# Performance work log

Hardware: AMD Instinct MI355X
Metric: run time of the kernel (lower is better)

## Reference

```python
import jax, jax.numpy as jnp
import numpy as np

# module config (matches init_kwargs)
EMBED = 128; HEADS = 8; HEAD_DIM = EMBED // HEADS  # 16, power of 2
MODES = 16            # hardcoded in FuncSelfAttention
WS = 4                # window_size
SHIFT = 2             # shift_size
NSUB = 8              # n_sub (subdomain grid of the full image)
NW = (NSUB // WS) ** 2   # 4 windows per image
S = WS * WS              # 16 tokens (subdomains) per window
BATCH0 = 4; B = BATCH0 * NW  # 16
P = 32                # per-subdomain spatial resolution (needs P//2+1 >= MODES)
HID = 512             # LogCPB MLP hidden width (Swin-v2 style)


def win_decompose2d(x, nsx, nsy, ws):
    # x: [b, c, H, W] -> [(b*wx*wy), ws*ws, c, sh, sw]
    b, c, H, W = x.shape
    sh = H // nsx; sw = W // nsy
    wx = nsx // ws; wy = nsy // ws
    x = x.reshape(b, c, wx, ws, sh, wy, ws, sw)
    x = x.transpose(0, 2, 5, 3, 6, 1, 4, 7)  # b, wx, wy, qx, qy, c, sh, sw
    return x.reshape(b * wx * wy, ws * ws, c, sh, sw)


def win_recompose2d(x, nsx, nsy, ws):
    # inverse of win_decompose2d: [(b*wx*wy), ws*ws, c, sh, sw] -> [b, c, H, W]
    wx = nsx // ws; wy = nsy // ws
    Bn, s, c, sh, sw = x.shape
    b = Bn // (wx * wy)
    x = x.reshape(b, wx, wy, ws, ws, c, sh, sw)
    x = x.transpose(0, 5, 1, 3, 6, 2, 4, 7)
    return x.reshape(b, c, wx * ws * sh, wy * ws * sw)


def spectral_conv(x, wr, wi):
    # SimpleSpectralConv2d: rfft2 -> low-mode complex channel mixing -> irfft2
    # x: [b, s, cin, h, w]; wr/wi: [cin, cout, m, m]
    m = wr.shape[-1]
    h, w = x.shape[-2:]
    xf = jnp.fft.rfft2(x, axes=(-2, -1))                       # [b,s,cin,h,w//2+1]
    ym = jnp.einsum('bsixy,ioxy->bsoxy', xf[..., :m, :m], wr + 1j * wi)
    out_ft = jnp.zeros(x.shape[:2] + (wr.shape[1], h, w // 2 + 1), dtype=ym.dtype)
    out_ft = out_ft.at[..., :m, :m].set(ym)
    return jnp.fft.irfft2(out_ft, s=(h, w), axes=(-2, -1))


def log_cpb(ws, w1, b1, w2):
    # Swin-v2 style log-spaced continuous position bias MLP -> [heads, S, S]
    g = jnp.arange(ws)
    coords = jnp.stack(jnp.meshgrid(g, g, indexing='ij'), -1).reshape(-1, 2)  # [S,2]
    rel = (coords[:, None, :] - coords[None, :, :]).astype(jnp.float32)       # [S,S,2]
    rel = jnp.sign(rel) * jnp.log2(1.0 + jnp.abs(rel)) / jnp.log2(8.0) * 8.0
    hdn = jax.nn.relu(rel @ w1 + b1)
    return (hdn @ w2).transpose(2, 0, 1)


def _build_attn_mask():
    # Faithful port of the Swin shifted-window mask construction in __init__
    img = np.zeros((NSUB, NSUB), np.float32)
    sl = [slice(0, -WS), slice(-WS, -SHIFT), slice(-SHIFT, None)]
    cnt = 0
    for hs in sl:
        for ws_ in sl:
            img[hs, ws_] = cnt
            cnt += 1
    mw = img.reshape(NSUB // WS, WS, NSUB // WS, WS).transpose(0, 2, 1, 3).reshape(NW, S)
    diff = mw[:, None, :] - mw[:, :, None]
    m = np.where(diff != 0, -1e9, 0.0).astype(np.float32)      # -inf in torch; -1e9 for safe grads
    return np.broadcast_to(m[:, None, :, :], (NW, HEADS, S, S)).copy()


def setup_inputs():
    key = jax.random.key(0)
    ks = jax.random.split(key, 8)
    sc = 1.0 / EMBED
    return {
        'seq': jax.random.normal(ks[0], (B, S, EMBED, P, P), jnp.float32),
        'qkv_wr': jax.random.normal(ks[1], (EMBED, 3 * EMBED, MODES, MODES), jnp.float32) * sc,
        'qkv_wi': jax.random.normal(ks[2], (EMBED, 3 * EMBED, MODES, MODES), jnp.float32) * sc,
        'out_wr': jax.random.normal(ks[3], (EMBED, EMBED, MODES, MODES), jnp.float32) * sc,
        'out_wi': jax.random.normal(ks[4], (EMBED, EMBED, MODES, MODES), jnp.float32) * sc,
        'cpb_w1': jax.random.normal(ks[5], (2, HID), jnp.float32) * 0.1,
        'cpb_b1': jnp.zeros((HID,), jnp.float32),
        'cpb_w2': jax.random.normal(ks[6], (HID, HEADS), jnp.float32) * 0.05,
        'attn_mask': jnp.asarray(_build_attn_mask()),
    }


def reference(seq, qkv_wr, qkv_wi, out_wr, out_wi, cpb_w1, cpb_b1, cpb_w2, attn_mask):
    Bn, s, C, h, w = seq.shape
    ssx = w // WS; ssy = h // WS  # subdomain_size per code: seq.size(-1)//n_sub_x with n_sub_x=window_size
    # shift: recompose windows to images, roll, decompose back
    x = win_recompose2d(seq, WS, WS, WS)
    x = jnp.roll(x, (-SHIFT * ssx, -SHIFT * ssy), axis=(-2, -1))
    x = win_decompose2d(x, WS, WS, WS)
    # qkv = spectral conv + residual tiling (v.repeat with dims[2]=3)
    qkv = spectral_conv(x, qkv_wr, qkv_wi) + jnp.concatenate([x, x, x], axis=2)
    qkv = qkv.reshape(Bn, s, 3, HEADS, HEAD_DIM, h, w)
    q = qkv[:, :, 0].transpose(0, 2, 1, 3, 4, 5)  # [B, H, s, d, h, w]
    k = qkv[:, :, 1].transpose(0, 2, 1, 3, 4, 5)
    v = qkv[:, :, 2].transpose(0, 2, 1, 3, 4, 5)
    bias = attn_mask + log_cpb(WS, cpb_w1, cpb_b1, cpb_w2)[None]  # [nW, H, S, S]
    # 'reimann' scores: Riemann-sum (mean over grid) inner product of q_i, k_j functions
    scale = 1.0 / ((h * w) * jnp.sqrt(jnp.float32(HEAD_DIM)))
    scores = jnp.einsum('bnidxy,bnjdxy->bnij', q, k) * scale      # [B, H, S, S]
    scores = scores.reshape(Bn // NW, NW, HEADS, s, s) + bias[None]
    attn = jax.nn.softmax(scores, axis=-1).reshape(Bn, HEADS, s, s)
    sa = jnp.einsum('bnij,bnjdxy->bnidxy', attn, v)               # [B, H, S, d, h, w]
    sa = sa.transpose(0, 2, 1, 3, 4, 5).reshape(Bn, s, C, h, w)   # _flatten
    sa = spectral_conv(sa, out_wr, out_wi)
    # un-shift
    sa = win_recompose2d(sa, WS, WS, WS)
    sa = jnp.roll(sa, (SHIFT * ssx, SHIFT * ssy), axis=(-2, -1))
    return win_decompose2d(sa, WS, WS, WS)
```

## Files before the change

### kernel.cpp

```cpp
#include <hip/hip_runtime.h>
#include <hip/hip_bf16.h>
#include <math.h>


#define DEVI __device__ __forceinline__
typedef unsigned short u16;
typedef unsigned int u32;
typedef __attribute__((ext_vector_type(8))) short short8;
typedef __attribute__((ext_vector_type(4))) float f32x4;

DEVI u16 f2b(float f) {
  union { __hip_bfloat16 h; u16 u; } cv;
  cv.h = __float2bfloat16(f);
  return cv.u;
}
DEVI float b2f(u16 u) { return __uint_as_float(((u32)u) << 16); }

__global__ __launch_bounds__(256) void k_bias(
    const float* __restrict__ w1, const float* __restrict__ b1,
    const float* __restrict__ w2, const float* __restrict__ amask,
    float* __restrict__ biasb) {
  __shared__ float w1s[1024];
  __shared__ float b1s[512];
  __shared__ float w2s[4096];
  int t = threadIdx.x;
  for (int k = t; k < 1024; k += 256) w1s[k] = w1[k];
  for (int k = t; k < 512; k += 256) b1s[k] = b1[k];
  for (int k = t; k < 4096; k += 256) w2s[k] = w2[k];
  __syncthreads();
  int i = t >> 4, j = t & 15;
  float r0 = (float)((i >> 2) - (j >> 2));
  float r1 = (float)((i & 3) - (j & 3));
  const float sc = 8.0f / 3.0f;
  float f0 = (r0 == 0.f) ? 0.f : copysignf(log2f(1.f + fabsf(r0)) * sc, r0);
  float f1 = (r1 == 0.f) ? 0.f : copysignf(log2f(1.f + fabsf(r1)) * sc, r1);
  float o[8];
#pragma unroll
  for (int h = 0; h < 8; h++) o[h] = 0.f;
  for (int k = 0; k < 512; k++) {
    float hd = f0 * w1s[k] + f1 * w1s[512 + k] + b1s[k];
    hd = fmaxf(hd, 0.f);
#pragma unroll
    for (int h = 0; h < 8; h++) o[h] += hd * w2s[k * 8 + h];
  }
  for (int w = 0; w < 4; w++)
#pragma unroll
    for (int h = 0; h < 8; h++) {
      int idx = ((w * 8 + h) * 16 + i) * 16 + j;
      biasb[idx] = amask[idx] + o[h];
    }
}

__global__ __launch_bounds__(256) void k_transpose_wb(
    const float* __restrict__ wr, const float* __restrict__ wi,
    ushort2* __restrict__ dst, int N) {
  __shared__ ushort2 ld[256][17];
  int t = threadIdx.x;
  int ob = blockIdx.x * 16;
  int cb = blockIdx.y * 8;
  for (int cc = 0; cc < 8; cc++) {
    int c = cb + cc;
    for (int oo = 0; oo < 16; oo++) {
      size_t si = ((size_t)c * N + ob + oo) * 256 + t;
      ushort2 u;
      u.x = f2b(wr[si]);
      u.y = f2b(wi[si]);
      ld[t][oo] = u;
    }
    __syncthreads();
    {
      int oo = t & 15, tq = t >> 4;
#pragma unroll
      for (int mr = 0; mr < 16; mr++) {
        int m = mr * 16 + tq;
        dst[((size_t)m * 128 + c) * N + ob + oo] = ld[m][oo];
      }
    }
    __syncthreads();
  }
}

template <int N>
__global__ __launch_bounds__(256) void k_build_b(
    const ushort2* __restrict__ Ws1, u16* __restrict__ Bt) {
  __shared__ ushort2 tile[128][65];
  int t = threadIdx.x;
  int ob = blockIdx.x;
  int m = blockIdx.y;
  {
    int c4 = t >> 6, o = t & 63;
    for (int cc = 0; cc < 32; cc++) {
      int c = cc * 4 + c4;
      tile[c][o] = Ws1[((size_t)m * 128 + c) * N + ob * 64 + o];
    }
  }
  __syncthreads();
  int l = t & 63, w2 = t >> 6;
  for (int rr = 0; rr < 32; rr++) {
    int r = w2 * 32 + rr;
    int ol = r >> 1, p = r & 1;
    size_t rowoff = ((size_t)m * (2 * N) + (size_t)ob * 128 + r) * 256;
#pragma unroll
    for (int ch = 0; ch < 2; ch++) {
      int c = ch * 64 + l;
      ushort2 wv = tile[c][ol];
      ushort2 u;
      u.x = p ? wv.y : wv.x;
      u.y = p ? wv.x : (u16)(wv.y ^ 0x8000);
      *(ushort2*)(Bt + rowoff + 2 * c) = u;
    }
  }
}

__global__ __launch_bounds__(256) void k_build_wdft(u16* __restrict__ Wdft) {
  int n = blockIdx.x;
  int m = n >> 1, q = n & 1;
  int kx = m >> 4, ky = m & 15;
  int t = threadIdx.x;
#pragma unroll
  for (int i = 0; i < 4; i++) {
    int p = i * 256 + t;
    int u = p >> 5, v = p & 31;
    int ph = (kx * u + ky * v) & 31;
    float th = 6.283185307179586f * (float)ph / 32.f;
    float sv, cv;
    sincosf(th, &sv, &cv);
    Wdft[(size_t)n * 1024 + p] = f2b(q ? -sv : cv);
  }
}

__global__ __launch_bounds__(256) void k_build_widft(u16* __restrict__ Widf) {
  int p = blockIdx.x;
  int x = p >> 5, y = p & 31;
  for (int n = threadIdx.x; n < 512; n += 256) {
    int m = n >> 1, q = n & 1;
    int kx = m >> 4, ky = m & 15;
    int ph = (kx * x + ky * y) & 31;
    float th = 6.283185307179586f * (float)ph / 32.f;
    float sv, cv;
    sincosf(th, &sv, &cv);
    float cky = (ky == 0) ? (1.f / 1024.f) : (2.f / 1024.f);
    Widf[(size_t)p * 512 + n] = f2b(q ? -sv * cky : cv * cky);
  }
}

__global__ __launch_bounds__(256) void k_gather(
    const float* __restrict__ seq, u16* __restrict__ Tbf) {
  int t = threadIdx.x;
  int cq = blockIdx.x;
  int bs = blockIdx.y;
  int b = bs >> 4, s = bs & 15;
  int qx = s >> 2, qy = s & 3;
  int u = t >> 3, vb = (t & 7) * 4;
  int uu = u + 16;
  int u2 = uu & 31;
  int qx2 = (qx + (uu >> 5)) & 3;
  int vv = vb + 16;
  int v2 = vv & 31;
  int qy2 = (qy + (vv >> 5)) & 3;
  int s2 = qx2 * 4 + qy2;
  size_t srcbase = (((size_t)(b * 16 + s2) * 128) << 10) + u2 * 32 + v2;
  size_t dstbase = (((size_t)bs * 128) << 10) + u * 32 + vb;
  for (int cc = 0; cc < 32; cc++) {
    size_t coff = (size_t)(cq * 32 + cc) << 10;
    float4 v = *(const float4*)(seq + srcbase + coff);
    ushort4 o;
    o.x = f2b(v.x);
    o.y = f2b(v.y);
    o.z = f2b(v.z);
    o.w = f2b(v.w);
    *(ushort4*)(Tbf + dstbase + coff) = o;
  }
}

__global__ __launch_bounds__(512) void k_dftm(
    const u16* __restrict__ Wdft, const u16* __restrict__ Tbf,
    u16* __restrict__ Xbf) {
  __shared__ char lds[49152];
  char* As = lds;
  char* Bs = lds + 32768;
  u16* st = (u16*)lds;
  int t = threadIdx.x;
  int mt = blockIdx.x, bs = blockIdx.y;
  int l = t & 63, w = t >> 6;
  int wm = w >> 1, wn = w & 1;
  f32x4 acc[4][4];
#pragma unroll
  for (int a_ = 0; a_ < 4; a_++)
#pragma unroll
    for (int b_ = 0; b_ < 4; b_++) acc[a_][b_] = (f32x4){0.f, 0.f, 0.f, 0.f};
  const u16* Ab = Wdft + (size_t)mt * 256 * 1024;
  const u16* Bb = Tbf + (size_t)bs * 128 * 1024;
  int srow = t >> 3, ss = t & 7;
  uint4 ra[4], rb[2];
#pragma unroll
  for (int i = 0; i < 4; i++)
    ra[i] = *(const uint4*)(Ab + (size_t)(i * 64 + srow) * 1024 + ss * 8);
#pragma unroll
  for (int i = 0; i < 2; i++)
    rb[i] = *(const uint4*)(Bb + (size_t)(i * 64 + srow) * 1024 + ss * 8);
  for (int kt = 0; kt < 16; kt++) {
    if (kt) __syncthreads();
#pragma unroll
    for (int i = 0; i < 4; i++) {
      int row = i * 64 + srow;
      *(uint4*)(As + row * 128 + ((ss ^ (row & 7)) << 4)) = ra[i];
    }
#pragma unroll
    for (int i = 0; i < 2; i++) {
      int row = i * 64 + srow;
      *(uint4*)(Bs + row * 128 + ((ss ^ (row & 7)) << 4)) = rb[i];
    }
    if (kt < 15) {
#pragma unroll
      for (int i = 0; i < 4; i++)
        ra[i] = *(const uint4*)(Ab + (size_t)(i * 64 + srow) * 1024 +
                                (kt + 1) * 64 + ss * 8);
#pragma unroll
      for (int i = 0; i < 2; i++)
        rb[i] = *(const uint4*)(Bb + (size_t)(i * 64 + srow) * 1024 +
                                (kt + 1) * 64 + ss * 8);
    }
    __syncthreads();
#pragma unroll
    for (int kk = 0; kk < 2; kk++) {
      short8 af[4], bg[4];
#pragma unroll
      for (int fm = 0; fm < 4; fm++) {
        int row = wm * 64 + fm * 16 + (l & 15);
        int chunk = kk * 4 + (l >> 4);
        af[fm] = *(const short8*)(As + row * 128 + ((chunk ^ (row & 7)) << 4));
      }
#pragma unroll
      for (int fn = 0; fn < 4; fn++) {
        int row = wn * 64 + fn * 16 + (l & 15);
        int chunk = kk * 4 + (l >> 4);
        bg[fn] = *(const short8*)(Bs + row * 128 + ((chunk ^ (row & 7)) << 4));
      }
#pragma unroll
      for (int fm = 0; fm < 4; fm++)
#pragma unroll
        for (int fn = 0; fn < 4; fn++)
          acc[fm][fn] = __builtin_amdgcn_mfma_f32_16x16x32_bf16(
              af[fm], bg[fn], acc[fm][fn], 0, 0, 0);
    }
  }
  int cr = (l >> 4) * 4, ccol = l & 15;
  for (int pass = 0; pass < 2; pass++) {
    __syncthreads();
    if ((wm >> 1) == pass) {
#pragma unroll
      for (int fm = 0; fm < 4; fm++) {
#pragma unroll
        for (int fn = 0; fn < 4; fn++) {
          int c = wn * 64 + fn * 16 + ccol;
#pragma unroll
          for (int rp = 0; rp < 4; rp += 2) {
            int rloc = (wm & 1) * 32 + fm * 8 + ((cr + rp) >> 1);
            ushort2 ub;
            ub.x = f2b(acc[fm][fn][rp]);
            ub.y = f2b(acc[fm][fn][rp + 1]);
            *(ushort2*)(st + rloc * 264 + 2 * c) = ub;
          }
        }
      }
    }
    __syncthreads();
#pragma unroll
    for (int it = 0; it < 4; it++) {
      int idx = it * 512 + t;
      int row = idx >> 5;
      int ch = idx & 31;
      uint4 v = *(const uint4*)(st + row * 264 + ch * 8);
      int m = mt * 128 + pass * 64 + row;
      *(uint4*)(Xbf + ((size_t)m * 256 + bs) * 256 + ch * 8) = v;
    }
  }
}

__global__ __launch_bounds__(64) void k_gram_mfma(
    const u16* __restrict__ Tbf, float* __restrict__ Gpart) {
  int dc = blockIdx.x;
  int bh = blockIdx.y;
  int b = bh >> 3, h = bh & 7;
  int l = threadIdx.x;
  f32x4 a0 = (f32x4){0.f, 0.f, 0.f, 0.f};
  f32x4 a1 = (f32x4){0.f, 0.f, 0.f, 0.f};
  const u16* base =
      Tbf + ((size_t)(b * 16 + (l & 15)) * 128 + h * 16 + dc * 4) * 1024;
  int ko = (l >> 4) * 8;
  for (int kk = 0; kk < 128; kk += 2) {
    short8 f0 = *(const short8*)(base + kk * 32 + ko);
    short8 f1 = *(const short8*)(base + kk * 32 + 32 + ko);
    a0 = __builtin_amdgcn_mfma_f32_16x16x32_bf16(f0, f0, a0, 0, 0, 0);
    a1 = __builtin_amdgcn_mfma_f32_16x16x32_bf16(f1, f1, a1, 0, 0, 0);
  }
  float* dst = Gpart + ((size_t)(dc * 16 + b) * 8 + h) * 256;
#pragma unroll
  for (int r = 0; r < 4; r++)
    dst[((l >> 4) * 4 + r) * 16 + (l & 15)] = a0[r] + a1[r];
}

template <int NP>
__global__ __launch_bounds__(512) void k_mixm(
    const u16* __restrict__ A, const u16* __restrict__ Bm,
    u16* __restrict__ Cb) {
  __shared__ char lds[65536];
  char* As = lds;
  char* Bs = lds + 32768;
  u16* st = (u16*)lds;
  int t = threadIdx.x;
  const int gx = NP / 256;
  int orig = blockIdx.y * gx + blockIdx.x;
  const int tot = gx * 256;
  int lid = (orig & 7) * (tot >> 3) + (orig >> 3);
  int nt = lid % gx;
  int m = lid / gx;
  int l = t & 63, w = t >> 6;
  int wm = w >> 1, wn = w & 1;
  f32x4 acc[4][8];
#pragma unroll
  for (int a_ = 0; a_ < 4; a_++)
#pragma unroll
    for (int b_ = 0; b_ < 8; b_++) acc[a_][b_] = (f32x4){0.f, 0.f, 0.f, 0.f};
  const u16* Ab = A + (size_t)m * 256 * 256;
  const u16* Bb = Bm + ((size_t)m * NP + nt * 256) * 256;
  int srow = t >> 3, ss = t & 7;
  uint4 ra[4], rb[4];
#pragma unroll
  for (int i = 0; i < 4; i++) {
    int row = i * 64 + srow;
    ra[i] = *(const uint4*)(Ab + (size_t)row * 256 + ss * 8);
    rb[i] = *(const uint4*)(Bb + (size_t)row * 256 + ss * 8);
  }
  for (int kt = 0; kt < 4; kt++) {
    if (kt) __syncthreads();
#pragma unroll
    for (int i = 0; i < 4; i++) {
      int row = i * 64 + srow;
      int sw = ((ss ^ (row & 7)) << 4);
      *(uint4*)(As + row * 128 + sw) = ra[i];
      *(uint4*)(Bs + row * 128 + sw) = rb[i];
    }
    if (kt < 3) {
#pragma unroll
      for (int i = 0; i < 4; i++) {
        int row = i * 64 + srow;
        ra[i] =
            *(const uint4*)(Ab + (size_t)row * 256 + (kt + 1) * 64 + ss * 8);
        rb[i] =
            *(const uint4*)(Bb + (size_t)row * 256 + (kt + 1) * 64 + ss * 8);
      }
    }
    __syncthreads();
#pragma unroll
    for (int kk = 0; kk < 2; kk++) {
      short8 af[4], bg[8];
#pragma unroll
      for (int fm = 0; fm < 4; fm++) {
        int row = wm * 64 + fm * 16 + (l & 15);
        int chunk = kk * 4 + (l >> 4);
        af[fm] = *(const short8*)(As + row * 128 + ((chunk ^ (row & 7)) << 4));
      }
#pragma unroll
      for (int fn = 0; fn < 8; fn++) {
        int row = wn * 128 + fn * 16 + (l & 15);
        int chunk = kk * 4 + (l >> 4);
        bg[fn] = *(const short8*)(Bs + row * 128 + ((chunk ^ (row & 7)) << 4));
      }
#pragma unroll
      for (int fm = 0; fm < 4; fm++)
#pragma unroll
        for (int fn = 0; fn < 8; fn++)
          acc[fm][fn] = __builtin_amdgcn_mfma_f32_16x16x32_bf16(
              bg[fn], af[fm], acc[fm][fn], 0, 0, 0);
    }
  }
#pragma unroll
  for (int fm = 0; fm < 4; fm++) {
    __syncthreads();
    int rloc = wm * 16 + (l & 15);
#pragma unroll
    for (int fn = 0; fn < 8; fn++) {
      int col = wn * 128 + fn * 16 + (l >> 4) * 4;
      ushort4 u;
      u.x = f2b(acc[fm][fn][0]);
      u.y = f2b(acc[fm][fn][1]);
      u.z = f2b(acc[fm][fn][2]);
      u.w = f2b(acc[fm][fn][3]);
      *(ushort4*)(st + rloc * 264 + col) = u;
    }
    __syncthreads();
#pragma unroll
    for (int it = 0; it < 4; it++) {
      int idx = it * 512 + t;
      int row = idx >> 5;
      int ch = idx & 31;
      uint4 v = *(const uint4*)(st + row * 264 + ch * 8);
      int bs = (row >> 4) * 64 + fm * 16 + (row & 15);
      *(uint4*)(Cb + ((size_t)m * 256 + bs) * NP + nt * 256 + ch * 8) = v;
    }
  }
}

__global__ __launch_bounds__(256) void k_transp_out(
    const ushort2* __restrict__ OUTb2, ushort2* __restrict__ OUTt2) {
  __shared__ ushort2 ld[128][129];
  int t = threadIdx.x;
  int bs = blockIdx.x;
  for (int mh = 0; mh < 2; mh++) {
    if (mh) __syncthreads();
    {
      int cidx = t & 127;
      int rb = t >> 7;
      for (int pass = 0; pass < 64; pass++) {
        int r = pass * 2 + rb;
        ld[r][cidx] = OUTb2[((size_t)(mh * 128 + r) * 256 + bs) * 128 + cidx];
      }
    }
    __syncthreads();
    {
      int ml = t & 127;
      int cb = t >> 7;
      for (int pass = 0; pass < 64; pass++) {
        int c = pass * 2 + cb;
        OUTt2[((size_t)bs * 128 + c) * 256 + mh * 128 + ml] = ld[ml][c];
      }
    }
  }
}

__global__ __launch_bounds__(512) void k_irfftm(
    const u16* __restrict__ Widf, const u16* __restrict__ OUTt,
    float* __restrict__ tmp) {
  __shared__ char lds[65536];
  char* As = lds;
  char* Bs = lds + 32768;
  float* stg = (float*)lds;
  int t = threadIdx.x;
  int ph = blockIdx.x, bs = blockIdx.y;
  int l = t & 63, w = t >> 6;
  int wm = w >> 1, wn = w & 1;
  f32x4 acc[4][4];
#pragma unroll
  for (int a_ = 0; a_ < 4; a_++)
#pragma unroll
    for (int b_ = 0; b_ < 4; b_++) acc[a_][b_] = (f32x4){0.f, 0.f, 0.f, 0.f};
  const u16* Ab = Widf + (size_t)ph * 256 * 512;
  const u16* Bb = OUTt + (size_t)bs * 128 * 512;
  int srow = t >> 3, ss = t & 7;
  uint4 ra[4], rb[2];
#pragma unroll
  for (int i = 0; i < 4; i++)
    ra[i] = *(const uint4*)(Ab + (size_t)(i * 64 + srow) * 512 + ss * 8);
#pragma unroll
  for (int i = 0; i < 2; i++)
    rb[i] = *(const uint4*)(Bb + (size_t)(i * 64 + srow) * 512 + ss * 8);
  for (int kt = 0; kt < 8; kt++) {
    if (kt) __syncthreads();
#pragma unroll
    for (int i = 0; i < 4; i++) {
      int row = i * 64 + srow;
      *(uint4*)(As + row * 128 + ((ss ^ (row & 7)) << 4)) = ra[i];
    }
#pragma unroll
    for (int i = 0; i < 2; i++) {
      int row = i * 64 + srow;
      *(uint4*)(Bs + row * 128 + ((ss ^ (row & 7)) << 4)) = rb[i];
    }
    if (kt < 7) {
#pragma unroll
      for (int i = 0; i < 4; i++)
        ra[i] = *(const uint4*)(Ab + (size_t)(i * 64 + srow) * 512 +
                                (kt + 1) * 64 + ss * 8);
#pragma unroll
      for (int i = 0; i < 2; i++)
        rb[i] = *(const uint4*)(Bb + (size_t)(i * 64 + srow) * 512 +
                                (kt + 1) * 64 + ss * 8);
    }
    __syncthreads();
#pragma unroll
    for (int kk = 0; kk < 2; kk++) {
      short8 wf[4], bg[4];
#pragma unroll
      for (int fm = 0; fm < 4; fm++) {
        int row = wm * 64 + fm * 16 + (l & 15);
        int chunk = kk * 4 + (l >> 4);
        wf[fm] = *(const short8*)(As + row * 128 + ((chunk ^ (row & 7)) << 4));
      }
#pragma unroll
      for (int fn = 0; fn < 4; fn++) {
        int row = wn * 64 + fn * 16 + (l & 15);
        int chunk = kk * 4 + (l >> 4);
        bg[fn] = *(const short8*)(Bs + row * 128 + ((chunk ^ (row & 7)) << 4));
      }
#pragma unroll
      for (int fm = 0; fm < 4; fm++)
#pragma unroll
        for (int fn = 0; fn < 4; fn++)
          acc[fm][fn] = __builtin_amdgcn_mfma_f32_16x16x32_bf16(
              wf[fm], bg[fn], acc[fm][fn], 0, 0, 0);
    }
  }
  for (int fmp = 0; fmp < 2; fmp++) {
    __syncthreads();
#pragma unroll
    for (int s = 0; s < 2; s++) {
      int fm = fmp * 2 + s;
#pragma unroll
      for (int fn = 0; fn < 4; fn++) {
        int c = wn * 64 + fn * 16 + (l & 15);
        int row = c * 4 + wm;
        int chunk = (s * 4 + (l >> 4)) ^ (c & 7);
        *(float4*)(stg + (row * 8 + chunk) * 4) =
            make_float4(acc[fm][fn][0], acc[fm][fn][1], acc[fm][fn][2],
                        acc[fm][fn][3]);
      }
    }
    __syncthreads();
#pragma unroll
    for (int it = 0; it < 8; it++) {
      int ci = it * 512 + t;
      int row = ci >> 3, k = ci & 7;
      int c = row >> 2, wm2 = row & 3;
      float4 v = *(const float4*)(stg + (row * 8 + (k ^ (c & 7))) * 4);
      int p0 = ph * 256 + wm2 * 64 + fmp * 32 + k * 4;
      *(float4*)(tmp + (((size_t)(bs * 128 + c)) << 10) + p0) = v;
    }
  }
}

__global__ __launch_bounds__(256) void k_unshift(
    const float* __restrict__ tmp, float* __restrict__ out) {
  int t = threadIdx.x;
  int cq = blockIdx.x;
  int bs2 = blockIdx.y;
  int b = bs2 >> 4, s2 = bs2 & 15;
  int qx2 = s2 >> 2, qy2 = s2 & 3;
  int v2 = (t & 7) * 4;
  int y, qy;
  if (v2 < 16) {
    y = v2 + 16;
    qy = (qy2 + 3) & 3;
  } else {
    y = v2 - 16;
    qy = qy2;
  }
  for (int it = 0; it < 32; it++) {
    int row = it * 32 + (t >> 3);
    int c = cq * 32 + (row >> 5);
    int u2 = row & 31;
    int x, qx;
    if (u2 < 16) {
      x = u2 + 16;
      qx = (qx2 + 3) & 3;
    } else {
      x = u2 - 16;
      qx = qx2;
    }
    int bs_src = b * 16 + qx * 4 + qy;
    float4 v = *(const float4*)(tmp + (((size_t)(bs_src * 128 + c)) << 10) +
                                x * 32 + y);
    *(float4*)(out + (((size_t)(bs2 * 128 + c)) << 10) + u2 * 32 + v2) = v;
  }
}

__global__ __launch_bounds__(256) void k_scores(
    const ushort2* __restrict__ Xb2, const ushort2* __restrict__ QKVmb,
    float* __restrict__ Spart) {
  __shared__ float2 Xs[16][17], Qs[16][17], Ks[16][17];
  int t = threadIdx.x;
  int mc = blockIdx.x;
  int bh = blockIdx.y;
  int b = bh >> 3, h = bh & 7;
  int i = t >> 4, j = t & 15;
  int bs = b * 16 + i;
  int d = j;
  int m0 = mc * 32;
  size_t xoff = ((size_t)m0 * 256 + bs) * 128 + h * 16 + d;
  size_t qoff = ((size_t)m0 * 256 + bs) * 384 + h * 16 + d;
  ushort2 ux = Xb2[xoff];
  ushort2 uq = QKVmb[qoff];
  ushort2 uk = QKVmb[qoff + 128];
  float acc = 0.f;
  for (int mm = 0; mm < 32; mm++) {
    int m = m0 + mm;
    Xs[i][d] = make_float2(b2f(ux.x), b2f(ux.y));
    Qs[i][d] = make_float2(b2f(uq.x), b2f(uq.y));
    Ks[i][d] = make_float2(b2f(uk.x), b2f(uk.y));
    __syncthreads();
    if (mm < 31) {
      ux = Xb2[xoff + (size_t)(mm + 1) * 32768];
      uq = QKVmb[qoff + (size_t)(mm + 1) * 98304];
      uk = QKVmb[qoff + (size_t)(mm + 1) * 98304 + 128];
    }
    int ky = m & 15, kx = m >> 4;
    if (ky > 0) {
#pragma unroll
      for (int dd = 0; dd < 16; dd++) {
        float2 Xi = Xs[i][dd], Qi = Qs[i][dd], Xj = Xs[j][dd], Kj = Ks[j][dd];
        float qr = Xi.x + Qi.x, qi = Xi.y + Qi.y;
        float kr = Xj.x + Kj.x, ki = Xj.y + Kj.y;
        acc += 2.f * (qr * kr + qi * ki - (Xi.x * Xj.x + Xi.y * Xj.y));
      }
    } else {
#pragma unroll
      for (int dd = 0; dd < 16; dd++) {
        float2 Xi = Xs[i][dd], Qi = Qs[i][dd], Xj = Xs[j][dd], Kj = Ks[j][dd];
        float cr = Xi.x * Kj.x + Xi.y * Kj.y + Qi.x * Xj.x + Qi.y * Xj.y;
        float qk =
            (kx == 0) ? (Qi.x * Kj.x) : 0.5f * (Qi.x * Kj.x + Qi.y * Kj.y);
        acc += cr + qk;
      }
    }
    __syncthreads();
  }
  Spart[((size_t)mc * 128 + bh) * 256 + t] = acc;
}

__global__ __launch_bounds__(256) void k_softmax(
    const float* __restrict__ Spart, const float* __restrict__ Gpart,
    const float* __restrict__ biasb, float* __restrict__ attn) {
  int t = threadIdx.x;
  int bh = blockIdx.x;
  int b = bh >> 3, h = bh & 7;
  int i = t >> 4, j = t & 15;
  float acc = 0.f;
#pragma unroll
  for (int mc = 0; mc < 8; mc++)
    acc += Spart[((size_t)mc * 128 + bh) * 256 + t];
  float G = 0.f;
#pragma unroll
  for (int dc = 0; dc < 4; dc++)
    G += Gpart[((size_t)(dc * 16 + b) * 8 + h) * 256 + t];
  float score = G * (1.f / 4096.f) + acc * (1.f / 4194304.f) +
                biasb[(((b & 3) * 8 + h) * 16 + i) * 16 + j];
  float mx = score;
#pragma unroll
  for (int o = 8; o >= 1; o >>= 1) mx = fmaxf(mx, __shfl_xor(mx, o, 16));
  float e = expf(score - mx);
  float sm = e;
#pragma unroll
  for (int o = 8; o >= 1; o >>= 1) sm += __shfl_xor(sm, o, 16);
  attn[(size_t)bh * 256 + t] = e / sm;
}

__global__ __launch_bounds__(256) void k_sav(
    const ushort2* __restrict__ Xb2, const ushort2* __restrict__ QKVmb,
    const float* __restrict__ attn, ushort2* __restrict__ SAfb) {
  __shared__ float at[8][16][17];
  __shared__ float2 vt[16][130];
  int t = threadIdx.x;
  int mc = blockIdx.x;
  int b = blockIdx.y;
  {
    int h = t >> 5, ii = (t >> 1) & 15, jb = (t & 1) * 8;
#pragma unroll
    for (int k = 0; k < 8; k++)
      at[h][ii][jb + k] = attn[((size_t)(b * 8 + h) * 16 + ii) * 16 + jb + k];
  }
  __syncthreads();
  int i = t >> 4, cg = t & 15;
  for (int mm = 0; mm < 16; mm++) {
    int m = mc * 16 + mm;
    int ky = m & 15, kx = m >> 4;
    {
      int jj = t >> 4;
      size_t row = (size_t)m * 256 + b * 16 + jj;
#pragma unroll
      for (int u = 0; u < 8; u++) {
        int c = cg + u * 16;
        ushort2 uv = QKVmb[row * 384 + 256 + c];
        float2 vm = make_float2(b2f(uv.x), b2f(uv.y));
        ushort2 uxv = Xb2[row * 128 + c];
        float2 xv = make_float2(b2f(uxv.x), b2f(uxv.y));
        float2 vh;
        if (ky == 0) {
          if (kx == 0)
            vh = make_float2(xv.x + vm.x, xv.y);
          else
            vh = make_float2(xv.x + 0.5f * vm.x, xv.y + 0.5f * vm.y);
        } else
          vh = make_float2(xv.x + vm.x, xv.y + vm.y);
        vt[jj][c] = vh;
      }
    }
    __syncthreads();
    float2 o8[8];
#pragma unroll
    for (int u = 0; u < 8; u++) o8[u] = make_float2(0.f, 0.f);
#pragma unroll
    for (int jj = 0; jj < 16; jj++) {
#pragma unroll
      for (int u = 0; u < 8; u++) {
        float av = at[u][i][jj];
        float2 v = vt[jj][cg + u * 16];
        o8[u].x += av * v.x;
        o8[u].y += av * v.y;
      }
    }
    size_t orow = (size_t)m * 256 + b * 16 + i;
#pragma unroll
    for (int u = 0; u < 8; u++) {
      ushort2 ub;
      ub.x = f2b(o8[u].x);
      ub.y = f2b(o8[u].y);
      SAfb[orow * 128 + cg + u * 16] = ub;
    }
    __syncthreads();
  }
}

extern "C" void kernel_launch(void* const* d_in, const int* in_sizes, int n_in,
                              void* d_out, int out_size, void* d_ws,
                              size_t ws_size, hipStream_t stream) {
  (void)in_sizes;
  (void)n_in;
  const float* seq = (const float*)d_in[0];
  const float* qwr = (const float*)d_in[1];
  const float* qwi = (const float*)d_in[2];
  const float* owr = (const float*)d_in[3];
  const float* owi = (const float*)d_in[4];
  const float* cw1 = (const float*)d_in[5];
  const float* cb1 = (const float*)d_in[6];
  const float* cw2 = (const float*)d_in[7];
  const float* amask = (const float*)d_in[8];
  float* out = (float*)d_out;
  char* ws = (char*)d_ws;

  const size_t R = 100663296;
  ushort2* Wq_s1b = (ushort2*)ws;
  u16* Tbf = (u16*)ws;
  u16* Xbf = (u16*)(ws + 67108864);
  ushort2* Xb2 = (ushort2*)Xbf;
  u16* Wob = (u16*)ws;
  ushort2* QKVmb = (ushort2*)(ws + R);
  u16* OUTb = (u16*)(ws + R);
  u16* OUTt = (u16*)(ws + R + 33554432);
  float* tmpb = (float*)(ws + R + 2 * 33554432);
  u16* Wqb = (u16*)(ws + 2 * R);
  ushort2* SAfb = (ushort2*)(ws + 2 * R);
  ushort2* Wo_s1b = (ushort2*)(ws + 3 * R);
  char* sm = ws + 3 * R + 16777216 + 67108864;
  u16* Wdft = (u16*)sm;
  float* Gpart = (float*)(sm + 1048576);
  float* biasb = (float*)(sm + 1572864);
  float* attn = (float*)(sm + 1605632);
  float* Spart = (float*)(sm + 1736704);
  u16* Widf = (u16*)(sm + 2785280);
  size_t need = 3 * R + 16777216 + 67108864 + 2785280 + 1048576;

  if (ws_size < need) {
    hipMemsetAsync(d_out, 0, (size_t)out_size * 4, stream);
    return;
  }

  dim3 blk(256);
  k_transpose_wb<<<dim3(24, 16), blk, 0, stream>>>(qwr, qwi, Wq_s1b, 384);
  k_build_b<384><<<dim3(6, 256), blk, 0, stream>>>(Wq_s1b, Wqb);
  k_transpose_wb<<<dim3(8, 16), blk, 0, stream>>>(owr, owi, Wo_s1b, 128);
  k_bias<<<dim3(1), blk, 0, stream>>>(cw1, cb1, cw2, amask, biasb);
  k_build_wdft<<<dim3(512), blk, 0, stream>>>(Wdft);
  k_build_widft<<<dim3(1024), blk, 0, stream>>>(Widf);
  k_gather<<<dim3(4, 256), blk, 0, stream>>>(seq, Tbf);
  k_dftm<<<dim3(2, 256), dim3(512), 0, stream>>>(Wdft, Tbf, Xbf);
  k_gram_mfma<<<dim3(4, 128), dim3(64), 0, stream>>>(Tbf, Gpart);
  k_mixm<768><<<dim3(3, 256), dim3(512), 0, stream>>>(Xbf, Wqb, (u16*)QKVmb);
  k_scores<<<dim3(8, 128), blk, 0, stream>>>(Xb2, QKVmb, Spart);
  k_softmax<<<dim3(128), blk, 0, stream>>>(Spart, Gpart, biasb, attn);
  k_build_b<128><<<dim3(2, 256), blk, 0, stream>>>(Wo_s1b, Wob);
  k_sav<<<dim3(16, 16), blk, 0, stream>>>(Xb2, QKVmb, attn, SAfb);
  k_mixm<256><<<dim3(1, 256), dim3(512), 0, stream>>>((const u16*)SAfb, Wob,
                                                      OUTb);
  k_transp_out<<<dim3(256), blk, 0, stream>>>((const ushort2*)OUTb,
                                              (ushort2*)OUTt);
  k_irfftm<<<dim3(4, 256), dim3(512), 0, stream>>>(Widf, OUTt, tmpb);
  k_unshift<<<dim3(4, 256), blk, 0, stream>>>(tmpb, out);
}
```

Before: 820.8 us.

## Relayout intermediate buffers: split Q/K/V planes, token-major X/SA, channel-last irfft output

Changes the memory layout of several intermediates. The DFT output X and the SA buffer become token-major, the QKV mix output is split into separate Q, K and V planes, and the irfft temp buffer becomes channel-last. k_unshift is rewritten to transpose through shared memory, and the consumers' address arithmetic is updated to match. The aim is better coalescing or locality in the scores, sav and unshift kernels. In exchange, some writes now become strided, and k_unshift runs on a single-dimension grid with an LDS transpose.

```diff
diff --git a/kernel.cpp b/kernel.cpp
--- a/kernel.cpp
+++ b/kernel.cpp
@@ -273,7 +273,7 @@
       int ch = idx & 31;
       uint4 v = *(const uint4*)(st + row * 264 + ch * 8);
       int m = mt * 128 + pass * 64 + row;
-      *(uint4*)(Xbf + ((size_t)m * 256 + bs) * 256 + ch * 8) = v;
+      *(uint4*)(Xbf + ((size_t)bs * 256 + m) * 256 + ch * 8) = v;
     }
   }
 }
@@ -323,14 +323,13 @@
   for (int a_ = 0; a_ < 4; a_++)
 #pragma unroll
     for (int b_ = 0; b_ < 8; b_++) acc[a_][b_] = (f32x4){0.f, 0.f, 0.f, 0.f};
-  const u16* Ab = A + (size_t)m * 256 * 256;
   const u16* Bb = Bm + ((size_t)m * NP + nt * 256) * 256;
   int srow = t >> 3, ss = t & 7;
   uint4 ra[4], rb[4];
 #pragma unroll
   for (int i = 0; i < 4; i++) {
     int row = i * 64 + srow;
-    ra[i] = *(const uint4*)(Ab + (size_t)row * 256 + ss * 8);
+    ra[i] = *(const uint4*)(A + ((size_t)row * 256 + m) * 256 + ss * 8);
     rb[i] = *(const uint4*)(Bb + (size_t)row * 256 + ss * 8);
   }
   for (int kt = 0; kt < 4; kt++) {
@@ -346,8 +345,8 @@
 #pragma unroll
       for (int i = 0; i < 4; i++) {
         int row = i * 64 + srow;
-        ra[i] =
-            *(const uint4*)(Ab + (size_t)row * 256 + (kt + 1) * 64 + ss * 8);
+        ra[i] = *(const uint4*)(A + ((size_t)row * 256 + m) * 256 +
+                                (kt + 1) * 64 + ss * 8);
         rb[i] =
             *(const uint4*)(Bb + (size_t)row * 256 + (kt + 1) * 64 + ss * 8);
       }
@@ -398,7 +397,8 @@
       int ch = idx & 31;
       uint4 v = *(const uint4*)(st + row * 264 + ch * 8);
       int bs = (row >> 4) * 64 + fm * 16 + (row & 15);
-      *(uint4*)(Cb + ((size_t)m * 256 + bs) * NP + nt * 256 + ch * 8) = v;
+      *(uint4*)(Cb + ((size_t)nt * 65536 + (size_t)m * 256 + bs) * 256 +
+                ch * 8) = v;
     }
   }
 }
@@ -502,72 +502,81 @@
               wf[fm], bg[fn], acc[fm][fn], 0, 0, 0);
     }
   }
-  for (int fmp = 0; fmp < 2; fmp++) {
-    __syncthreads();
-#pragma unroll
-    for (int s = 0; s < 2; s++) {
-      int fm = fmp * 2 + s;
-#pragma unroll
-      for (int fn = 0; fn < 4; fn++) {
-        int c = wn * 64 + fn * 16 + (l & 15);
-        int row = c * 4 + wm;
-        int chunk = (s * 4 + (l >> 4)) ^ (c & 7);
-        *(float4*)(stg + (row * 8 + chunk) * 4) =
-            make_float4(acc[fm][fn][0], acc[fm][fn][1], acc[fm][fn][2],
-                        acc[fm][fn][3]);
+  for (int pass = 0; pass < 2; pass++) {
+    __syncthreads();
+    if ((wm >> 1) == pass) {
+#pragma unroll
+      for (int fm = 0; fm < 4; fm++) {
+#pragma unroll
+        for (int fn = 0; fn < 4; fn++) {
+          int c = wn * 64 + fn * 16 + (l & 15);
+#pragma unroll
+          for (int r = 0; r < 4; r++) {
+            int pl = (wm & 1) * 64 + fm * 16 + (l >> 4) * 4 + r;
+            stg[pl * 128 + (((c >> 2) ^ (pl & 7)) << 2) + (c & 3)] =
+                acc[fm][fn][r];
+          }
+        }
       }
     }
     __syncthreads();
 #pragma unroll
     for (int it = 0; it < 8; it++) {
       int ci = it * 512 + t;
-      int row = ci >> 3, k = ci & 7;
-      int c = row >> 2, wm2 = row & 3;
-      float4 v = *(const float4*)(stg + (row * 8 + (k ^ (c & 7))) * 4);
-      int p0 = ph * 256 + wm2 * 64 + fmp * 32 + k * 4;
-      *(float4*)(tmp + (((size_t)(bs * 128 + c)) << 10) + p0) = v;
+      int prow = ci >> 5, ch = ci & 31;
+      float4 v = *(const float4*)(stg + prow * 128 + ((ch ^ (prow & 7)) << 2));
+      int p = ph * 256 + pass * 128 + prow;
+      *(float4*)(tmp + ((size_t)bs * 1024 + p) * 128 + ch * 4) = v;
     }
   }
 }
 
 __global__ __launch_bounds__(256) void k_unshift(
     const float* __restrict__ tmp, float* __restrict__ out) {
-  int t = threadIdx.x;
-  int cq = blockIdx.x;
-  int bs2 = blockIdx.y;
+  __shared__ float ld[2][32][132];
+  int t = threadIdx.x;
+  int bs2 = blockIdx.x;
   int b = bs2 >> 4, s2 = bs2 & 15;
   int qx2 = s2 >> 2, qy2 = s2 & 3;
-  int v2 = (t & 7) * 4;
-  int y, qy;
-  if (v2 < 16) {
-    y = v2 + 16;
-    qy = (qy2 + 3) & 3;
-  } else {
-    y = v2 - 16;
-    qy = qy2;
-  }
-  for (int it = 0; it < 32; it++) {
-    int row = it * 32 + (t >> 3);
-    int c = cq * 32 + (row >> 5);
-    int u2 = row & 31;
-    int x, qx;
-    if (u2 < 16) {
-      x = u2 + 16;
-      qx = (qx2 + 3) & 3;
-    } else {
-      x = u2 - 16;
-      qx = qx2;
-    }
-    int bs_src = b * 16 + qx * 4 + qy;
-    float4 v = *(const float4*)(tmp + (((size_t)(bs_src * 128 + c)) << 10) +
-                                x * 32 + y);
-    *(float4*)(out + (((size_t)(bs2 * 128 + c)) << 10) + u2 * 32 + v2) = v;
+  for (int u2 = 0; u2 < 32; u2++) {
+    int cu = u2 & 1;
+    int x = (u2 < 16) ? u2 + 16 : u2 - 16;
+    int qx = (u2 < 16) ? (qx2 + 3) & 3 : qx2;
+    {
+      int r = t >> 3;
+      int y = (r < 16) ? r + 16 : r - 16;
+      int qy = (r < 16) ? (qy2 + 3) & 3 : qy2;
+      int bs_src = b * 16 + qx * 4 + qy;
+      const float* src = tmp + ((size_t)bs_src * 1024 + x * 32 + y) * 128;
+#pragma unroll
+      for (int k = 0; k < 4; k++) {
+        int c4 = (t & 7) + 8 * k;
+        float4 v = *(const float4*)(src + c4 * 4);
+        ld[cu][r][c4 * 4 + 0] = v.x;
+        ld[cu][r][c4 * 4 + 1] = v.y;
+        ld[cu][r][c4 * 4 + 2] = v.z;
+        ld[cu][r][c4 * 4 + 3] = v.w;
+      }
+    }
+    __syncthreads();
+    {
+      int c = t >> 1, vh = (t & 1) * 16;
+      float* dst = out + (((size_t)bs2 * 128 + c) << 10) + u2 * 32 + vh;
+#pragma unroll
+      for (int k = 0; k < 4; k++) {
+        float4 v = make_float4(ld[cu][vh + k * 4 + 0][c],
+                               ld[cu][vh + k * 4 + 1][c],
+                               ld[cu][vh + k * 4 + 2][c],
+                               ld[cu][vh + k * 4 + 3][c]);
+        *(float4*)(dst + k * 4) = v;
+      }
+    }
   }
 }
 
 __global__ __launch_bounds__(256) void k_scores(
-    const ushort2* __restrict__ Xb2, const ushort2* __restrict__ QKVmb,
-    float* __restrict__ Spart) {
+    const ushort2* __restrict__ Xb2, const ushort2* __restrict__ Qb2,
+    const ushort2* __restrict__ Kb2, float* __restrict__ Spart) {
   __shared__ float2 Xs[16][17], Qs[16][17], Ks[16][17];
   int t = threadIdx.x;
   int mc = blockIdx.x;
@@ -577,11 +586,11 @@
   int bs = b * 16 + i;
   int d = j;
   int m0 = mc * 32;
-  size_t xoff = ((size_t)m0 * 256 + bs) * 128 + h * 16 + d;
-  size_t qoff = ((size_t)m0 * 256 + bs) * 384 + h * 16 + d;
+  size_t xoff = ((size_t)bs * 256 + m0) * 128 + h * 16 + d;
+  size_t qoff = ((size_t)m0 * 256 + bs) * 128 + h * 16 + d;
   ushort2 ux = Xb2[xoff];
-  ushort2 uq = QKVmb[qoff];
-  ushort2 uk = QKVmb[qoff + 128];
+  ushort2 uq = Qb2[qoff];
+  ushort2 uk = Kb2[qoff];
   float acc = 0.f;
   for (int mm = 0; mm < 32; mm++) {
     int m = m0 + mm;
@@ -590,9 +599,9 @@
     Ks[i][d] = make_float2(b2f(uk.x), b2f(uk.y));
     __syncthreads();
     if (mm < 31) {
-      ux = Xb2[xoff + (size_t)(mm + 1) * 32768];
-      uq = QKVmb[qoff + (size_t)(mm + 1) * 98304];
-      uk = QKVmb[qoff + (size_t)(mm + 1) * 98304 + 128];
+      ux = Xb2[xoff + (size_t)(mm + 1) * 128];
+      uq = Qb2[qoff + (size_t)(mm + 1) * 32768];
+      uk = Kb2[qoff + (size_t)(mm + 1) * 32768];
     }
     int ky = m & 15, kx = m >> 4;
     if (ky > 0) {
@@ -646,7 +655,7 @@
 }
 
 __global__ __launch_bounds__(256) void k_sav(
-    const ushort2* __restrict__ Xb2, const ushort2* __restrict__ QKVmb,
+    const ushort2* __restrict__ Xb2, const ushort2* __restrict__ Vb2,
     const float* __restrict__ attn, ushort2* __restrict__ SAfb) {
   __shared__ float at[8][16][17];
   __shared__ float2 vt[16][130];
@@ -666,13 +675,14 @@
     int ky = m & 15, kx = m >> 4;
     {
       int jj = t >> 4;
-      size_t row = (size_t)m * 256 + b * 16 + jj;
+      size_t vrow = ((size_t)m * 256 + b * 16 + jj) * 128;
+      size_t xrow = ((size_t)(b * 16 + jj) * 256 + m) * 128;
 #pragma unroll
       for (int u = 0; u < 8; u++) {
         int c = cg + u * 16;
-        ushort2 uv = QKVmb[row * 384 + 256 + c];
+        ushort2 uv = Vb2[vrow + c];
         float2 vm = make_float2(b2f(uv.x), b2f(uv.y));
-        ushort2 uxv = Xb2[row * 128 + c];
+        ushort2 uxv = Xb2[xrow + c];
         float2 xv = make_float2(b2f(uxv.x), b2f(uxv.y));
         float2 vh;
         if (ky == 0) {
@@ -699,13 +709,13 @@
         o8[u].y += av * v.y;
       }
     }
-    size_t orow = (size_t)m * 256 + b * 16 + i;
+    size_t orow = ((size_t)(b * 16 + i) * 256 + m) * 128;
 #pragma unroll
     for (int u = 0; u < 8; u++) {
       ushort2 ub;
       ub.x = f2b(o8[u].x);
       ub.y = f2b(o8[u].y);
-      SAfb[orow * 128 + cg + u * 16] = ub;
+      SAfb[orow + cg + u * 16] = ub;
     }
     __syncthreads();
   }
@@ -734,7 +744,10 @@
   u16* Xbf = (u16*)(ws + 67108864);
   ushort2* Xb2 = (ushort2*)Xbf;
   u16* Wob = (u16*)ws;
-  ushort2* QKVmb = (ushort2*)(ws + R);
+  u16* QKV = (u16*)(ws + R);
+  ushort2* Qb2 = (ushort2*)QKV;
+  ushort2* Kb2 = Qb2 + 8388608;
+  ushort2* Vb2 = Qb2 + 16777216;
   u16* OUTb = (u16*)(ws + R);
   u16* OUTt = (u16*)(ws + R + 33554432);
   float* tmpb = (float*)(ws + R + 2 * 33554432);
@@ -765,15 +778,15 @@
   k_gather<<<dim3(4, 256), blk, 0, stream>>>(seq, Tbf);
   k_dftm<<<dim3(2, 256), dim3(512), 0, stream>>>(Wdft, Tbf, Xbf);
   k_gram_mfma<<<dim3(4, 128), dim3(64), 0, stream>>>(Tbf, Gpart);
-  k_mixm<768><<<dim3(3, 256), dim3(512), 0, stream>>>(Xbf, Wqb, (u16*)QKVmb);
-  k_scores<<<dim3(8, 128), blk, 0, stream>>>(Xb2, QKVmb, Spart);
+  k_mixm<768><<<dim3(3, 256), dim3(512), 0, stream>>>(Xbf, Wqb, QKV);
+  k_scores<<<dim3(8, 128), blk, 0, stream>>>(Xb2, Qb2, Kb2, Spart);
   k_softmax<<<dim3(128), blk, 0, stream>>>(Spart, Gpart, biasb, attn);
   k_build_b<128><<<dim3(2, 256), blk, 0, stream>>>(Wo_s1b, Wob);
-  k_sav<<<dim3(16, 16), blk, 0, stream>>>(Xb2, QKVmb, attn, SAfb);
+  k_sav<<<dim3(16, 16), blk, 0, stream>>>(Xb2, Vb2, attn, SAfb);
   k_mixm<256><<<dim3(1, 256), dim3(512), 0, stream>>>((const u16*)SAfb, Wob,
                                                       OUTb);
   k_transp_out<<<dim3(256), blk, 0, stream>>>((const ushort2*)OUTb,
                                               (ushort2*)OUTt);
   k_irfftm<<<dim3(4, 256), dim3(512), 0, stream>>>(Widf, OUTt, tmpb);
-  k_unshift<<<dim3(4, 256), blk, 0, stream>>>(tmpb, out);
-}
+  k_unshift<<<dim3(256), blk, 0, stream>>>(tmpb, out);
+}
```

Measured after the change: 838.3 us. +2.1%, slower.
